# Optimization experiments

Measured on AMD Instinct MI355X. Metric: run time of the kernel, lower is better.

## Reference

```python
import jax, jax.numpy as jnp
import numpy as np

N_NODES = 50000
N_EDGES = 600000
F_IN = 64
N_GRAPHS = 2000
OUT_DIM = 1
BN_EPS = 1e-5


def _bn(x, gamma, beta):
    # BatchNorm1d training-mode forward: biased batch stats over node/row dim
    m = jnp.mean(x, axis=0)
    v = jnp.var(x, axis=0)
    return (x - m) * jax.lax.rsqrt(v + BN_EPS) * gamma + beta


def _gcn(x, W, b, src, dst):
    # PyG GCNConv: h = x @ W; symmetric-normalized aggregation with self-loops; bias after agg
    n = x.shape[0]
    h = x @ W                                    # [N, C_out]
    ones = jnp.ones((src.shape[0],), h.dtype)
    deg = jax.ops.segment_sum(ones, dst, num_segments=n) + 1.0  # +1 self-loop
    dinv = jax.lax.rsqrt(deg)
    norm = (dinv[src] * dinv[dst])[:, None]      # [E, 1]
    agg = jax.ops.segment_sum(h[src] * norm, dst, num_segments=n)
    agg = agg + h * (1.0 / deg)[:, None]         # self-loop term: deg^{-1/2}*deg^{-1/2}
    return agg + b


def _pool_mean(x, batch, g):
    s = jax.ops.segment_sum(x, batch, num_segments=g)
    c = jax.ops.segment_sum(jnp.ones((x.shape[0],), x.dtype), batch, num_segments=g)
    return s / jnp.maximum(c, 1.0)[:, None]


def _forward(xc, xs, W1c, b1c, g1c, be1c, W2c, b2c, g2c, be2c,
             W1s, b1s, g1s, be1s, W2s, b2s, g2s, be2s,
             Wf1, bf1, gf1, bef1, Wf2, bf2,
             src_c, dst_c, src_s, dst_s, batch):
    hc = jax.nn.relu(_bn(_gcn(xc, W1c, b1c, src_c, dst_c), g1c, be1c))
    hc = jax.nn.relu(_bn(_gcn(hc, W2c, b2c, src_c, dst_c), g2c, be2c))
    hs = jax.nn.relu(_bn(_gcn(xs, W1s, b1s, src_s, dst_s), g1s, be1s))
    hs = jax.nn.relu(_bn(_gcn(hs, W2s, b2s, src_s, dst_s), g2s, be2s))
    pc = _pool_mean(hc, batch, N_GRAPHS)         # [G, 64]
    ps = _pool_mean(hs, batch, N_GRAPHS)         # [G, 64]
    h = jnp.concatenate([pc, ps], axis=1)        # [G, 128]
    h = jax.nn.relu(_bn(h @ Wf1 + bf1, gf1, bef1))  # dropout is identity in eval
    return h @ Wf2 + bf2                         # [G, OUT_DIM]


def setup_inputs() -> dict:
    key = jax.random.key(0)
    ks = jax.random.split(key, 16)

    def glorot(k, fan_in, fan_out):
        s = np.sqrt(2.0 / (fan_in + fan_out)).astype(np.float32)
        return jax.random.normal(k, (fan_in, fan_out), jnp.float32) * s

    inp = {
        'x_chromophore': jax.random.normal(ks[0], (N_NODES, F_IN), jnp.float32),
        'x_solvent': jax.random.normal(ks[1], (N_NODES, F_IN), jnp.float32),
        'edge_index_chromophore': jax.random.randint(ks[2], (2, N_EDGES), 0, N_NODES),
        'edge_index_solvent': jax.random.randint(ks[3], (2, N_EDGES), 0, N_NODES),
        'batch': jnp.sort(jax.random.randint(ks[4], (N_NODES,), 0, N_GRAPHS)),
        # chromophore branch params
        'W1c': glorot(ks[5], F_IN, 128), 'b1c': jnp.zeros((128,), jnp.float32),
        'g1c': jnp.ones((128,), jnp.float32), 'be1c': jnp.zeros((128,), jnp.float32),
        'W2c': glorot(ks[6], 128, 64), 'b2c': jnp.zeros((64,), jnp.float32),
        'g2c': jnp.ones((64,), jnp.float32), 'be2c': jnp.zeros((64,), jnp.float32),
        # solvent branch params
        'W1s': glorot(ks[7], F_IN, 128), 'b1s': jnp.zeros((128,), jnp.float32),
        'g1s': jnp.ones((128,), jnp.float32), 'be1s': jnp.zeros((128,), jnp.float32),
        'W2s': glorot(ks[8], 128, 64), 'b2s': jnp.zeros((64,), jnp.float32),
        'g2s': jnp.ones((64,), jnp.float32), 'be2s': jnp.zeros((64,), jnp.float32),
        # MLP head
        'Wf1': glorot(ks[9], 128, 64), 'bf1': jnp.zeros((64,), jnp.float32),
        'gf1': jnp.ones((64,), jnp.float32), 'bef1': jnp.zeros((64,), jnp.float32),
        'Wf2': glorot(ks[10], 64, OUT_DIM), 'bf2': jnp.zeros((OUT_DIM,), jnp.float32),
    }
    return inp


def reference(x_chromophore, x_solvent, edge_index_chromophore, edge_index_solvent, batch,
              W1c, b1c, g1c, be1c, W2c, b2c, g2c, be2c,
              W1s, b1s, g1s, be1s, W2s, b2s, g2s, be2s,
              Wf1, bf1, gf1, bef1, Wf2, bf2):
    src_c, dst_c = edge_index_chromophore[0], edge_index_chromophore[1]
    src_s, dst_s = edge_index_solvent[0], edge_index_solvent[1]
    return _forward(x_chromophore, x_solvent,
                    W1c, b1c, g1c, be1c, W2c, b2c, g2c, be2c,
                    W1s, b1s, g1s, be1s, W2s, b2s, g2s, be2s,
                    Wf1, bf1, gf1, bef1, Wf2, bf2,
                    src_c, dst_c, src_s, dst_s, batch)
```

## Files before the change

### kernel.cpp

```cpp
#include <hip/hip_runtime.h>
#include <hip/hip_bf16.h>
#include <cstdint>
#include <cstddef>

#define NN 50000
#define NE 600000
#define NG 2000
#define NBUCK 49
#define SLOTS 16
#define NCHUNK 3125

typedef __attribute__((ext_vector_type(8))) short bf8;
typedef __attribute__((ext_vector_type(4))) float f32x4;

__device__ __forceinline__ unsigned short f2bf(float f) {
    uint32_t u = __float_as_uint(f);
    uint32_t r = (u + 0x7FFFu + ((u >> 16) & 1u)) >> 16;
    return (unsigned short)r;
}
__device__ __forceinline__ float bf2f(unsigned short h) {
    return __uint_as_float(((uint32_t)h) << 16);
}

__global__ __launch_bounds__(256) void conv_bf16_kernel(const float* __restrict__ x0,
                                                        const float* __restrict__ x1,
                                                        unsigned short* __restrict__ out) {
    int b = blockIdx.y;
    const float* x = b ? x1 : x0;
    unsigned short* o = out + (size_t)b * NN * 64;
    int i = (blockIdx.x * 256 + threadIdx.x) * 4;
    if (i + 3 < NN * 64) {
        float4 v = *(const float4*)&x[i];
        ushort4 r = make_ushort4(f2bf(v.x), f2bf(v.y), f2bf(v.z), f2bf(v.w));
        *(ushort4*)&o[i] = r;
    }
}

template<int K, int N>
__global__ __launch_bounds__(256) void pack_w(const float* __restrict__ W0,
                                              const float* __restrict__ W1,
                                              unsigned short* __restrict__ out) {
    int b = blockIdx.y;
    const float* W = b ? W1 : W0;
    unsigned short* o = out + (size_t)b * K * N;
    int idx = blockIdx.x * 256 + threadIdx.x;
    const int total = (N / 16) * (K / 32) * 64;
    if (idx >= total) return;
    int l = idx & 63;
    int th = idx >> 6;
    int h = th % (K / 32);
    int t = th / (K / 32);
    int col = t * 16 + (l & 15);
    int k0 = h * 32 + (l >> 4) * 8;
    ushort4 lo = make_ushort4(f2bf(W[(k0 + 0) * N + col]), f2bf(W[(k0 + 1) * N + col]),
                              f2bf(W[(k0 + 2) * N + col]), f2bf(W[(k0 + 3) * N + col]));
    ushort4 hi = make_ushort4(f2bf(W[(k0 + 4) * N + col]), f2bf(W[(k0 + 5) * N + col]),
                              f2bf(W[(k0 + 6) * N + col]), f2bf(W[(k0 + 7) * N + col]));
    *(ushort4*)&o[idx * 8] = lo;
    *(ushort4*)&o[idx * 8 + 4] = hi;
}

__global__ __launch_bounds__(256) void bucket_hist(const int* __restrict__ d0,
                                                   const int* __restrict__ d1,
                                                   int* __restrict__ bucketCnt, int nE) {
    int b = blockIdx.y;
    const int* dst = b ? d1 : d0;
    __shared__ int h[NBUCK];
    for (int i = threadIdx.x; i < NBUCK; i += 256) h[i] = 0;
    __syncthreads();
    for (int e = blockIdx.x * 256 + threadIdx.x; e < nE; e += gridDim.x * 256)
        atomicAdd(&h[dst[e] >> 10], 1);
    __syncthreads();
    for (int i = threadIdx.x; i < NBUCK; i += 256)
        if (h[i]) atomicAdd(&bucketCnt[b * NBUCK + i], h[i]);
}

__global__ void bucket_scan(const int* __restrict__ bucketCnt,
                            int* __restrict__ bucketOff, int* __restrict__ bucketCur) {
    int b = threadIdx.x;
    if (b < 2) {
        int run = 0;
        for (int i = 0; i < NBUCK; ++i) {
            bucketOff[b * NBUCK + i] = run;
            bucketCur[b * NBUCK + i] = run;
            run += bucketCnt[b * NBUCK + i];
        }
    }
}

__global__ __launch_bounds__(256) void bucket_scatter(const int* __restrict__ s0,
                                                      const int* __restrict__ d0,
                                                      const int* __restrict__ s1,
                                                      const int* __restrict__ d1,
                                                      int* __restrict__ bucketCur,
                                                      uint32_t* __restrict__ bent, int nE) {
    int b = blockIdx.y;
    const int* src = b ? s1 : s0;
    const int* dst = b ? d1 : d0;
    __shared__ int cnt[NBUCK];
    __shared__ int base[NBUCK];
    const int tid = threadIdx.x;
    for (int i = tid; i < NBUCK; i += 256) cnt[i] = 0;
    __syncthreads();

    const int e0 = blockIdx.x * 2048 + tid;
    int bk[8], slot[8];
    uint32_t pay[8];
#pragma unroll
    for (int k = 0; k < 8; ++k) {
        int e = e0 + k * 256;
        if (e < nE) {
            int d = dst[e], s = src[e];
            bk[k] = d >> 10;
            pay[k] = ((uint32_t)(d & 1023) << 16) | (uint32_t)s;
            slot[k] = atomicAdd(&cnt[bk[k]], 1);
        } else bk[k] = -1;
    }
    __syncthreads();
    for (int i = tid; i < NBUCK; i += 256) {
        int c = cnt[i];
        base[i] = c ? atomicAdd(&bucketCur[b * NBUCK + i], c) : 0;
    }
    __syncthreads();
#pragma unroll
    for (int k = 0; k < 8; ++k)
        if (bk[k] >= 0)
            bent[(size_t)b * NE + base[bk[k]] + slot[k]] = pay[k];
}

__global__ __launch_bounds__(256) void csr_build(const uint32_t* __restrict__ bent,
                                                 const int* __restrict__ bucketOff,
                                                 const int* __restrict__ bucketCnt,
                                                 int* __restrict__ row_ptr,
                                                 float* __restrict__ dinv,
                                                 uint16_t* __restrict__ perm) {
    __shared__ int lcnt[1024];
    __shared__ int lcur[1024];
    __shared__ int sscan[256];
    const int bk = blockIdx.x;
    const int b = blockIdx.y;
    const int tid = threadIdx.x;
    const int ebase = bucketOff[b * NBUCK + bk];
    const int ecnt = bucketCnt[b * NBUCK + bk];
    const int node0 = bk << 10;
    const uint32_t* be = bent + (size_t)b * NE + ebase;
    int* rp = row_ptr + b * (NN + 1);
    float* dv = dinv + (size_t)b * NN;
    uint16_t* pm = perm + (size_t)b * NE + ebase;

    for (int i = tid; i < 1024; i += 256) lcnt[i] = 0;
    __syncthreads();
    for (int i = tid; i < ecnt; i += 256) atomicAdd(&lcnt[be[i] >> 16], 1);
    __syncthreads();

    int c[4], s = 0;
#pragma unroll
    for (int j = 0; j < 4; ++j) { c[j] = lcnt[tid * 4 + j]; s += c[j]; }
    sscan[tid] = s;
    __syncthreads();
    for (int off = 1; off < 256; off <<= 1) {
        int v = (tid >= off) ? sscan[tid - off] : 0;
        __syncthreads();
        sscan[tid] += v;
        __syncthreads();
    }
    int run = sscan[tid] - s;
#pragma unroll
    for (int j = 0; j < 4; ++j) {
        int nl = tid * 4 + j;
        int g = node0 + nl;
        if (g < NN) {
            rp[g] = ebase + run;
            lcur[nl] = run;
            dv[g] = rsqrtf((float)c[j] + 1.0f);
        }
        run += c[j];
    }
    if (bk == NBUCK - 1 && tid == 0) rp[NN] = ebase + ecnt;
    __syncthreads();

    for (int i = tid; i < ecnt; i += 256) {
        uint32_t en = be[i];
        int nl = en >> 16;
        int pos = atomicAdd(&lcur[nl], 1);
        pm[pos] = (uint16_t)(en & 0xFFFFu);
    }
}

__global__ __launch_bounds__(256) void weight_fill(const uint16_t* __restrict__ perm,
                                                   const float* __restrict__ dinv,
                                                   uint32_t* __restrict__ permw, int nE) {
    int b = blockIdx.y;
    const uint16_t* pm = perm + (size_t)b * NE;
    const float* dv = dinv + (size_t)b * NN;
    uint32_t* pw = permw + (size_t)b * NE;
    int i = (blockIdx.x * 256 + threadIdx.x) * 4;
    if (i + 3 < nE) {
        ushort4 s4 = *(const ushort4*)&pm[i];
        uint4 o;
        o.x = ((uint32_t)f2bf(dv[s4.x]) << 16) | (uint32_t)s4.x;
        o.y = ((uint32_t)f2bf(dv[s4.y]) << 16) | (uint32_t)s4.y;
        o.z = ((uint32_t)f2bf(dv[s4.z]) << 16) | (uint32_t)s4.z;
        o.w = ((uint32_t)f2bf(dv[s4.w]) << 16) | (uint32_t)s4.w;
        *(uint4*)&pw[i] = o;
    } else {
        for (; i < nE; ++i) {
            uint16_t s = pm[i];
            pw[i] = ((uint32_t)f2bf(dv[s]) << 16) | (uint32_t)s;
        }
    }
}

template<bool STATS>
__global__ __launch_bounds__(256) void gemm1_mfma(const unsigned short* __restrict__ Xbf,
                                                  const unsigned short* __restrict__ Wp,
                                                  unsigned short* __restrict__ Y,
                                                  float* __restrict__ sums) {
    __shared__ float ls[128], ls2[128];
    const int b = blockIdx.y;
    const unsigned short* __restrict__ X = Xbf + (size_t)b * NN * 64;
    const unsigned short* __restrict__ W = Wp + (size_t)b * 64 * 128;
    unsigned short* __restrict__ Yb = Y + (size_t)b * NN * 128;
    const int tid = threadIdx.x;
    const int w = tid >> 6, lane = tid & 63;
    if (STATS) {
        for (int i = tid; i < 128; i += 256) { ls[i] = 0.f; ls2[i] = 0.f; }
        __syncthreads();
    }
    const int chunk = blockIdx.x * 4 + w;
    const bool act = chunk < NCHUNK;
    const int m = lane & 15, quad = lane >> 4;

    if (act) {
        const int row = chunk * 16 + m;
        bf8 a0 = *(const bf8*)&X[(size_t)row * 64 + quad * 8];
        bf8 a1 = *(const bf8*)&X[(size_t)row * 64 + 32 + quad * 8];
        f32x4 acc[8];
#pragma unroll
        for (int t = 0; t < 8; ++t) acc[t] = (f32x4){0.f, 0.f, 0.f, 0.f};
#pragma unroll
        for (int t = 0; t < 8; ++t) {
            bf8 b0 = *(const bf8*)&W[((t * 2 + 0) * 64 + lane) * 8];
            bf8 b1 = *(const bf8*)&W[((t * 2 + 1) * 64 + lane) * 8];
            acc[t] = __builtin_amdgcn_mfma_f32_16x16x32_bf16(a0, b0, acc[t], 0, 0, 0);
            acc[t] = __builtin_amdgcn_mfma_f32_16x16x32_bf16(a1, b1, acc[t], 0, 0, 0);
        }
        const int rbase = chunk * 16 + quad * 4;
#pragma unroll
        for (int t = 0; t < 8; ++t) {
            float s = 0.f, s2 = 0.f;
#pragma unroll
            for (int r = 0; r < 4; ++r) {
                float v = acc[t][r];
                Yb[(size_t)(rbase + r) * 128 + t * 16 + m] = f2bf(v);
                s += v; s2 = fmaf(v, v, s2);
            }
            if (STATS) {
                atomicAdd(&ls[t * 16 + m], s);
                atomicAdd(&ls2[t * 16 + m], s2);
            }
        }
    }
    if (STATS) {
        __syncthreads();
        int slot = blockIdx.x & (SLOTS - 1);
        float* sb = sums + (size_t)(b * SLOTS + slot) * 256;
        if (tid < 128) {
            atomicAdd(&sb[tid], ls[tid]);
            atomicAdd(&sb[128 + tid], ls2[tid]);
        }
    }
}

__global__ __launch_bounds__(256) void gemm2_mfma(const unsigned short* __restrict__ H1,
                                                  const unsigned short* __restrict__ Wp,
                                                  const float* __restrict__ scale,
                                                  const float* __restrict__ shift,
                                                  unsigned short* __restrict__ Y) {
    const int b = blockIdx.y;
    const unsigned short* __restrict__ X = H1 + (size_t)b * NN * 128;
    const unsigned short* __restrict__ W = Wp + (size_t)b * 128 * 64;
    const float* sc = scale + b * 128;
    const float* sh = shift + b * 128;
    unsigned short* __restrict__ Yb = Y + (size_t)b * NN * 64;
    const int tid = threadIdx.x;
    const int w = tid >> 6, lane = tid & 63;
    const int chunk = blockIdx.x * 4 + w;
    if (chunk >= NCHUNK) return;
    const int m = lane & 15, quad = lane >> 4;
    const int row = chunk * 16 + m;

    f32x4 acc[4];
#pragma unroll
    for (int t = 0; t < 4; ++t) acc[t] = (f32x4){0.f, 0.f, 0.f, 0.f};
#pragma unroll
    for (int h = 0; h < 4; ++h) {
        const int k0 = h * 32 + quad * 8;
        bf8 araw = *(const bf8*)&X[(size_t)row * 128 + k0];
        float4 sc0 = *(const float4*)&sc[k0];
        float4 sc1 = *(const float4*)&sc[k0 + 4];
        float4 sh0 = *(const float4*)&sh[k0];
        float4 sh1 = *(const float4*)&sh[k0 + 4];
        float scv[8] = {sc0.x, sc0.y, sc0.z, sc0.w, sc1.x, sc1.y, sc1.z, sc1.w};
        float shv[8] = {sh0.x, sh0.y, sh0.z, sh0.w, sh1.x, sh1.y, sh1.z, sh1.w};
        bf8 af;
#pragma unroll
        for (int j = 0; j < 8; ++j) {
            float v = bf2f((unsigned short)araw[j]);
            v = fmaxf(fmaf(v, scv[j], shv[j]), 0.f);
            af[j] = (short)f2bf(v);
        }
#pragma unroll
        for (int t = 0; t < 4; ++t) {
            bf8 bf = *(const bf8*)&W[((t * 4 + h) * 64 + lane) * 8];
            acc[t] = __builtin_amdgcn_mfma_f32_16x16x32_bf16(af, bf, acc[t], 0, 0, 0);
        }
    }
    const int rbase = chunk * 16 + quad * 4;
#pragma unroll
    for (int t = 0; t < 4; ++t)
#pragma unroll
        for (int r = 0; r < 4; ++r)
            Yb[(size_t)(rbase + r) * 64 + t * 16 + m] = f2bf(acc[t][r]);
}

template<bool STATS>
__global__ __launch_bounds__(256) void agg2_kernel(const unsigned short* __restrict__ hall,
                                                   const int* __restrict__ row_ptr,
                                                   const uint32_t* __restrict__ permw,
                                                   const float* __restrict__ dinv,
                                                   float* __restrict__ out,
                                                   float* __restrict__ sums, int nNodes) {
    const int b = blockIdx.y;
    const unsigned short* __restrict__ h = hall + (size_t)b * NN * 64;
    const int* rp = row_ptr + b * (NN + 1);
    const uint32_t* pe = permw + (size_t)b * NE;
    const float* dv = dinv + (size_t)b * NN;
    float* ob = out + (size_t)b * nNodes * 64;

    const int wave = blockIdx.x * 4 + (threadIdx.x >> 6);
    const int lane = threadIdx.x & 63;
    float fin = 0.f;
    const bool active = wave < nNodes;
    if (active) {
        const int d = wave;
        const float di = dv[d];
        const int p0 = rp[d], p1 = rp[d + 1];
        float a = 0.f;
        for (int p = p0; p < p1; p += 8) {
            int idx[8]; float w[8];
#pragma unroll
            for (int k = 0; k < 8; ++k) {
                bool vld = (p + k) < p1;
                int pk = vld ? (p + k) : p;
                uint32_t en = pe[pk];
                idx[k] = (int)(en & 0xFFFFu);
                w[k] = vld ? bf2f((unsigned short)(en >> 16)) : 0.f;
            }
            float v[8];
#pragma unroll
            for (int k = 0; k < 8; ++k) v[k] = bf2f(h[(size_t)idx[k] * 64 + lane]);
#pragma unroll
            for (int k = 0; k < 8; ++k) a = fmaf(w[k], v[k], a);
        }
        float hd = bf2f(h[(size_t)d * 64 + lane]);
        fin = di * fmaf(di, hd, a);
        ob[(size_t)d * 64 + lane] = fin;
    }
    if constexpr (STATS) {
        __shared__ float ls[256], ls2[256];
        ls[threadIdx.x] = fin;
        ls2[threadIdx.x] = fin * fin;
        __syncthreads();
        if (threadIdx.x < 64) {
            float s  = ls[threadIdx.x] + ls[threadIdx.x + 64] + ls[threadIdx.x + 128] + ls[threadIdx.x + 192];
            float s2 = ls2[threadIdx.x] + ls2[threadIdx.x + 64] + ls2[threadIdx.x + 128] + ls2[threadIdx.x + 192];
            int slot = blockIdx.x & (SLOTS - 1);
            float* sb = sums + ((size_t)(b * SLOTS + slot) * 2) * 64;
            atomicAdd(&sb[threadIdx.x], s);
            atomicAdd(&sb[64 + threadIdx.x], s2);
        }
    }
}

__global__ void bn_finalize2_kernel(const float* __restrict__ sums, int C, float invN,
                                    const float* __restrict__ g0, const float* __restrict__ g1,
                                    const float* __restrict__ b0, const float* __restrict__ b1,
                                    float* __restrict__ scale, float* __restrict__ shift) {
    int b = blockIdx.y;
    int c = threadIdx.x;
    if (c >= C) return;
    float s = 0.f, s2 = 0.f;
    for (int k = 0; k < SLOTS; ++k) {
        const float* sb = sums + ((size_t)(b * SLOTS + k) * 2) * C;
        s += sb[c];
        s2 += sb[C + c];
    }
    const float* gamma = b ? g1 : g0;
    const float* beta = b ? b1 : b0;
    float m = s * invN;
    float var = s2 * invN - m * m;
    float sc = gamma[c] * rsqrtf(var + 1e-5f);
    scale[b * C + c] = sc;
    shift[b * C + c] = beta[c] - m * sc;
}

__global__ void bn_finalize_kernel(const float* __restrict__ sums, int C, float invN,
                                   const float* __restrict__ gamma, const float* __restrict__ beta,
                                   float* __restrict__ scale, float* __restrict__ shift) {
    int c = blockIdx.x * blockDim.x + threadIdx.x;
    if (c >= C) return;
    float m = sums[c] * invN;
    float var = sums[C + c] * invN - m * m;
    float sc = gamma[c] * rsqrtf(var + 1e-5f);
    scale[c] = sc;
    shift[c] = beta[c] - m * sc;
}

__global__ __launch_bounds__(64) void pool2_kernel(const float* __restrict__ x,
                                                   const float* __restrict__ scale,
                                                   const float* __restrict__ shift,
                                                   const int* __restrict__ batch,
                                                   float* __restrict__ Hmean, int n) {
    int b = blockIdx.y;
    const float* xb = x + (size_t)b * NN * 64;
    int g = blockIdx.x;
    int c = threadIdx.x;
    int lo = 0, hi = n;
    while (lo < hi) { int mid = (lo + hi) >> 1; if (batch[mid] < g) lo = mid + 1; else hi = mid; }
    int start = lo;
    hi = n;
    while (lo < hi) { int mid = (lo + hi) >> 1; if (batch[mid] <= g) lo = mid + 1; else hi = mid; }
    int end = lo;
    float s = 0.f;
    float sc = scale[b * 64 + c], sh = shift[b * 64 + c];
    for (int r = start; r < end; ++r)
        s += fmaxf(fmaf(xb[(size_t)r * 64 + c], sc, sh), 0.f);
    float cf = (float)(end - start);
    Hmean[(size_t)g * 128 + b * 64 + c] = s / fmaxf(cf, 1.f);
}

__global__ __launch_bounds__(64) void head_gemm1_kernel(const float* __restrict__ H,
                                                        const float* __restrict__ Wf1,
                                                        float* __restrict__ T) {
    __shared__ float row[128];
    int g = blockIdx.x;
    int c = threadIdx.x;
    row[c] = H[(size_t)g * 128 + c];
    row[c + 64] = H[(size_t)g * 128 + 64 + c];
    __syncthreads();
    float acc = 0.f;
#pragma unroll 8
    for (int k = 0; k < 128; ++k) acc = fmaf(row[k], Wf1[k * 64 + c], acc);
    T[(size_t)g * 64 + c] = acc;
}

__global__ __launch_bounds__(64) void head_final_kernel(const float* __restrict__ T,
                                                        const float* __restrict__ scale,
                                                        const float* __restrict__ shift,
                                                        const float* __restrict__ Wf2,
                                                        const float* __restrict__ bf2,
                                                        float* __restrict__ out) {
    int g = blockIdx.x;
    int c = threadIdx.x;
    float v = fmaxf(fmaf(T[(size_t)g * 64 + c], scale[c], shift[c]), 0.f) * Wf2[c];
#pragma unroll
    for (int off = 32; off > 0; off >>= 1) v += __shfl_down(v, off, 64);
    if (c == 0) out[g] = v + bf2[0];
}

template<int C>
__global__ __launch_bounds__(256) void bn_stats_kernel(const float* __restrict__ x, int n,
                                                       float* __restrict__ sums) {
    constexpr int RP = 256 / C;
    __shared__ float ls[256], ls2[256];
    int c = threadIdx.x % C;
    int sub = threadIdx.x / C;
    float s = 0.f, s2 = 0.f;
    for (int r = blockIdx.x * RP + sub; r < n; r += gridDim.x * RP) {
        float v = x[(size_t)r * C + c];
        s += v; s2 += v * v;
    }
    ls[threadIdx.x] = s; ls2[threadIdx.x] = s2;
    __syncthreads();
    if (sub == 0) {
#pragma unroll
        for (int k = 1; k < RP; ++k) { s += ls[k * C + c]; s2 += ls2[k * C + c]; }
        atomicAdd(&sums[c], s);
        atomicAdd(&sums[C + c], s2);
    }
}


static inline size_t alignup(size_t x) { return (x + 255) & ~(size_t)255; }

extern "C" void kernel_launch(void* const* d_in, const int* in_sizes, int n_in,
                              void* d_out, int out_size, void* d_ws, size_t ws_size,
                              hipStream_t stream) {
    const float* xc  = (const float*)d_in[0];
    const float* xs  = (const float*)d_in[1];
    const int*   eic = (const int*)d_in[2];
    const int*   eis = (const int*)d_in[3];
    const int*   batch = (const int*)d_in[4];
    const float* W1c = (const float*)d_in[5];
    const float* g1c = (const float*)d_in[7];
    const float* be1c = (const float*)d_in[8];
    const float* W2c = (const float*)d_in[9];
    const float* g2c = (const float*)d_in[11];
    const float* be2c = (const float*)d_in[12];
    const float* W1s = (const float*)d_in[13];
    const float* g1s = (const float*)d_in[15];
    const float* be1s = (const float*)d_in[16];
    const float* W2s = (const float*)d_in[17];
    const float* g2s = (const float*)d_in[19];
    const float* be2s = (const float*)d_in[20];
    const float* Wf1 = (const float*)d_in[21];
    const float* gf1 = (const float*)d_in[23];
    const float* bef1 = (const float*)d_in[24];
    const float* Wf2 = (const float*)d_in[25];
    const float* bf2 = (const float*)d_in[26];
    float* out = (float*)d_out;

    char* ws = (char*)d_ws;
    size_t off = 0;
    auto alloc = [&](size_t bytes) { char* p = ws + off; off += alignup(bytes); return p; };

    int*      bucketCnt = (int*)alloc(2 * NBUCK * 4);
    int*      bucketOff = (int*)alloc(2 * NBUCK * 4);
    int*      bucketCur = (int*)alloc(2 * NBUCK * 4);
    uint32_t* bent      = (uint32_t*)alloc((size_t)2 * NE * 4);
    uint16_t* perm      = (uint16_t*)alloc(((size_t)2 * NE + 64) * 2);
    int*      row_ptr   = (int*)alloc(2 * (NN + 1) * 4);
    float*    dinv      = (float*)alloc((size_t)2 * NN * 4);
    unsigned short* xbf   = (unsigned short*)alloc((size_t)2 * NN * 64 * 2);
    unsigned short* h1bf  = (unsigned short*)alloc((size_t)2 * NN * 128 * 2);
    unsigned short* h2bf  = (unsigned short*)alloc((size_t)2 * NN * 64 * 2);
    unsigned short* Wp1   = (unsigned short*)alloc((size_t)2 * 64 * 128 * 2);
    unsigned short* Wp2   = (unsigned short*)alloc((size_t)2 * 128 * 64 * 2);
    float*    aggx      = (float*)alloc((size_t)2 * NN * 64 * 4);
    float*    sums      = (float*)alloc((size_t)2 * SLOTS * 2 * 128 * 4);
    float*    hsums     = (float*)alloc(128 * 4);
    float*    bnscale   = (float*)alloc(2 * 128 * 4);
    float*    bnshift   = (float*)alloc(2 * 128 * 4);
    float*    Hmean     = (float*)alloc((size_t)NG * 128 * 4);
    float*    T         = (float*)alloc((size_t)NG * 64 * 4);

    const float invN = 1.0f / (float)NN;
    const size_t sumsBytes = (size_t)2 * SLOTS * 2 * 128 * 4;
    const int gemmBlocks = (NCHUNK + 3) / 4;

    conv_bf16_kernel<<<dim3((NN * 64 / 4 + 255) / 256, 2), 256, 0, stream>>>(xc, xs, xbf);
    pack_w<64, 128><<<dim3(4, 2), 256, 0, stream>>>(W1c, W1s, Wp1);
    pack_w<128, 64><<<dim3(4, 2), 256, 0, stream>>>(W2c, W2s, Wp2);

    hipMemsetAsync(bucketCnt, 0, 2 * NBUCK * 4, stream);
    bucket_hist<<<dim3(64, 2), 256, 0, stream>>>(eic + NE, eis + NE, bucketCnt, NE);
    bucket_scan<<<1, 64, 0, stream>>>(bucketCnt, bucketOff, bucketCur);
    bucket_scatter<<<dim3((NE + 2047) / 2048, 2), 256, 0, stream>>>(
        eic, eic + NE, eis, eis + NE, bucketCur, bent, NE);
    csr_build<<<dim3(NBUCK, 2), 256, 0, stream>>>(bent, bucketOff, bucketCnt,
                                                  row_ptr, dinv, perm);
    weight_fill<<<dim3((NE / 4 + 255) / 256, 2), 256, 0, stream>>>(perm, dinv, bent, NE);

    agg2_kernel<false><<<dim3((NN + 3) / 4, 2), 256, 0, stream>>>(
        xbf, row_ptr, bent, dinv, aggx, nullptr, NN);
    conv_bf16_kernel<<<dim3((NN * 64 / 4 + 255) / 256, 2), 256, 0, stream>>>(
        aggx, aggx + (size_t)NN * 64, xbf);
    hipMemsetAsync(sums, 0, sumsBytes, stream);
    gemm1_mfma<true><<<dim3(gemmBlocks, 2), 256, 0, stream>>>(xbf, Wp1, h1bf, sums);
    bn_finalize2_kernel<<<dim3(1, 2), 128, 0, stream>>>(sums, 128, invN,
                                                        g1c, g1s, be1c, be1s, bnscale, bnshift);

    gemm2_mfma<<<dim3(gemmBlocks, 2), 256, 0, stream>>>(h1bf, Wp2, bnscale, bnshift, h2bf);
    hipMemsetAsync(sums, 0, sumsBytes, stream);
    agg2_kernel<true><<<dim3((NN + 3) / 4, 2), 256, 0, stream>>>(
        h2bf, row_ptr, bent, dinv, aggx, sums, NN);
    bn_finalize2_kernel<<<dim3(1, 2), 64, 0, stream>>>(sums, 64, invN,
                                                       g2c, g2s, be2c, be2s, bnscale, bnshift);

    pool2_kernel<<<dim3(NG, 2), 64, 0, stream>>>(aggx, bnscale, bnshift, batch, Hmean, NN);

    head_gemm1_kernel<<<NG, 64, 0, stream>>>(Hmean, Wf1, T);
    hipMemsetAsync(hsums, 0, 128 * 4, stream);
    bn_stats_kernel<64><<<32, 256, 0, stream>>>(T, NG, hsums);
    bn_finalize_kernel<<<1, 64, 0, stream>>>(hsums, 64, 1.0f / (float)NG, gf1, bef1,
                                             bnscale, bnshift);
    head_final_kernel<<<NG, 64, 0, stream>>>(T, bnscale, bnshift, Wf2, bf2, out);
}
```

Baseline: 409.1 us.

## Vectorize edge aggregation with 4-edge lanes and write bf16 output directly

The aggregation kernel now has each 16-lane group handle one edge, loading 4 bf16 features per lane (8-byte loads), and reduces the partial sums across groups with shuffles. It writes bf16 output directly, which removes the separate fp32-to-bf16 conversion kernel and halves the aggregation output and pool input traffic. The BN stats memsets are merged into a single upfront memset, and the per-block reduction uses LDS atomics. Storing the second-layer aggregate in bf16 before BN and pooling adds rounding error.

After: 423.4 us. +3.5%, slower.

```diff
diff --git a/kernel.cpp b/kernel.cpp
--- a/kernel.cpp
+++ b/kernel.cpp
@@ -21,6 +21,8 @@
 __device__ __forceinline__ float bf2f(unsigned short h) {
     return __uint_as_float(((uint32_t)h) << 16);
 }
+__device__ __forceinline__ float bflo(uint32_t u) { return __uint_as_float(u << 16); }
+__device__ __forceinline__ float bfhi(uint32_t u) { return __uint_as_float(u & 0xFFFF0000u); }
 
 __global__ __launch_bounds__(256) void conv_bf16_kernel(const float* __restrict__ x0,
                                                         const float* __restrict__ x1,
@@ -325,60 +327,82 @@
 }
 
 template<bool STATS>
-__global__ __launch_bounds__(256) void agg2_kernel(const unsigned short* __restrict__ hall,
+__global__ __launch_bounds__(256) void agg3_kernel(const unsigned short* __restrict__ hall,
                                                    const int* __restrict__ row_ptr,
                                                    const uint32_t* __restrict__ permw,
                                                    const float* __restrict__ dinv,
-                                                   float* __restrict__ out,
+                                                   unsigned short* __restrict__ out,
                                                    float* __restrict__ sums, int nNodes) {
     const int b = blockIdx.y;
     const unsigned short* __restrict__ h = hall + (size_t)b * NN * 64;
     const int* rp = row_ptr + b * (NN + 1);
     const uint32_t* pe = permw + (size_t)b * NE;
     const float* dv = dinv + (size_t)b * NN;
-    float* ob = out + (size_t)b * nNodes * 64;
+    unsigned short* ob = out + (size_t)b * nNodes * 64;
 
     const int wave = blockIdx.x * 4 + (threadIdx.x >> 6);
     const int lane = threadIdx.x & 63;
-    float fin = 0.f;
+    const int g = lane >> 4;
+    const int li = lane & 15;
+    float fin0 = 0.f, fin1 = 0.f, fin2 = 0.f, fin3 = 0.f;
     const bool active = wave < nNodes;
     if (active) {
         const int d = wave;
         const float di = dv[d];
         const int p0 = rp[d], p1 = rp[d + 1];
-        float a = 0.f;
+        float a0 = 0.f, a1 = 0.f, a2 = 0.f, a3 = 0.f;
         for (int p = p0; p < p1; p += 8) {
-            int idx[8]; float w[8];
-#pragma unroll
-            for (int k = 0; k < 8; ++k) {
-                bool vld = (p + k) < p1;
-                int pk = vld ? (p + k) : p;
+#pragma unroll
+            for (int q = 0; q < 2; ++q) {
+                int pk = p + q * 4 + g;
+                bool vld = pk < p1;
+                pk = vld ? pk : p0;
                 uint32_t en = pe[pk];
-                idx[k] = (int)(en & 0xFFFFu);
-                w[k] = vld ? bf2f((unsigned short)(en >> 16)) : 0.f;
+                int idx = (int)(en & 0xFFFFu);
+                float w = vld ? bf2f((unsigned short)(en >> 16)) : 0.f;
+                uint2 hv = *(const uint2*)&h[(size_t)idx * 64 + li * 4];
+                a0 = fmaf(w, bflo(hv.x), a0);
+                a1 = fmaf(w, bfhi(hv.x), a1);
+                a2 = fmaf(w, bflo(hv.y), a2);
+                a3 = fmaf(w, bfhi(hv.y), a3);
             }
-            float v[8];
-#pragma unroll
-            for (int k = 0; k < 8; ++k) v[k] = bf2f(h[(size_t)idx[k] * 64 + lane]);
-#pragma unroll
-            for (int k = 0; k < 8; ++k) a = fmaf(w[k], v[k], a);
-        }
-        float hd = bf2f(h[(size_t)d * 64 + lane]);
-        fin = di * fmaf(di, hd, a);
-        ob[(size_t)d * 64 + lane] = fin;
+        }
+        uint2 hd = *(const uint2*)&h[(size_t)d * 64 + li * 4];
+        float ws = (g == 0) ? di : 0.f;
+        a0 = fmaf(ws, bflo(hd.x), a0);
+        a1 = fmaf(ws, bfhi(hd.x), a1);
+        a2 = fmaf(ws, bflo(hd.y), a2);
+        a3 = fmaf(ws, bfhi(hd.y), a3);
+        a0 += __shfl_xor(a0, 16, 64); a0 += __shfl_xor(a0, 32, 64);
+        a1 += __shfl_xor(a1, 16, 64); a1 += __shfl_xor(a1, 32, 64);
+        a2 += __shfl_xor(a2, 16, 64); a2 += __shfl_xor(a2, 32, 64);
+        a3 += __shfl_xor(a3, 16, 64); a3 += __shfl_xor(a3, 32, 64);
+        fin0 = di * a0; fin1 = di * a1; fin2 = di * a2; fin3 = di * a3;
+        if (g == 0) {
+            ushort4 st = make_ushort4(f2bf(fin0), f2bf(fin1), f2bf(fin2), f2bf(fin3));
+            *(ushort4*)&ob[(size_t)d * 64 + li * 4] = st;
+        }
     }
     if constexpr (STATS) {
-        __shared__ float ls[256], ls2[256];
-        ls[threadIdx.x] = fin;
-        ls2[threadIdx.x] = fin * fin;
+        __shared__ float ls[64], ls2[64];
+        if (threadIdx.x < 64) { ls[threadIdx.x] = 0.f; ls2[threadIdx.x] = 0.f; }
+        __syncthreads();
+        if (active && g == 0) {
+            atomicAdd(&ls[li * 4 + 0], fin0);
+            atomicAdd(&ls[li * 4 + 1], fin1);
+            atomicAdd(&ls[li * 4 + 2], fin2);
+            atomicAdd(&ls[li * 4 + 3], fin3);
+            atomicAdd(&ls2[li * 4 + 0], fin0 * fin0);
+            atomicAdd(&ls2[li * 4 + 1], fin1 * fin1);
+            atomicAdd(&ls2[li * 4 + 2], fin2 * fin2);
+            atomicAdd(&ls2[li * 4 + 3], fin3 * fin3);
+        }
         __syncthreads();
         if (threadIdx.x < 64) {
-            float s  = ls[threadIdx.x] + ls[threadIdx.x + 64] + ls[threadIdx.x + 128] + ls[threadIdx.x + 192];
-            float s2 = ls2[threadIdx.x] + ls2[threadIdx.x + 64] + ls2[threadIdx.x + 128] + ls2[threadIdx.x + 192];
             int slot = blockIdx.x & (SLOTS - 1);
             float* sb = sums + ((size_t)(b * SLOTS + slot) * 2) * 64;
-            atomicAdd(&sb[threadIdx.x], s);
-            atomicAdd(&sb[64 + threadIdx.x], s2);
+            atomicAdd(&sb[threadIdx.x], ls[threadIdx.x]);
+            atomicAdd(&sb[64 + threadIdx.x], ls2[threadIdx.x]);
         }
     }
 }
@@ -417,13 +441,13 @@
     shift[c] = beta[c] - m * sc;
 }
 
-__global__ __launch_bounds__(64) void pool2_kernel(const float* __restrict__ x,
+__global__ __launch_bounds__(64) void pool2_kernel(const unsigned short* __restrict__ x,
                                                    const float* __restrict__ scale,
                                                    const float* __restrict__ shift,
                                                    const int* __restrict__ batch,
                                                    float* __restrict__ Hmean, int n) {
     int b = blockIdx.y;
-    const float* xb = x + (size_t)b * NN * 64;
+    const unsigned short* xb = x + (size_t)b * NN * 64;
     int g = blockIdx.x;
     int c = threadIdx.x;
     int lo = 0, hi = n;
@@ -435,7 +459,7 @@
     float s = 0.f;
     float sc = scale[b * 64 + c], sh = shift[b * 64 + c];
     for (int r = start; r < end; ++r)
-        s += fmaxf(fmaf(xb[(size_t)r * 64 + c], sc, sh), 0.f);
+        s += fmaxf(fmaf(bf2f(xb[(size_t)r * 64 + c]), sc, sh), 0.f);
     float cf = (float)(end - start);
     Hmean[(size_t)g * 128 + b * 64 + c] = s / fmaxf(cf, 1.f);
 }
@@ -533,25 +557,28 @@
     int*      row_ptr   = (int*)alloc(2 * (NN + 1) * 4);
     float*    dinv      = (float*)alloc((size_t)2 * NN * 4);
     unsigned short* xbf   = (unsigned short*)alloc((size_t)2 * NN * 64 * 2);
+    unsigned short* aggbf = (unsigned short*)alloc((size_t)2 * NN * 64 * 2);
     unsigned short* h1bf  = (unsigned short*)alloc((size_t)2 * NN * 128 * 2);
     unsigned short* h2bf  = (unsigned short*)alloc((size_t)2 * NN * 64 * 2);
     unsigned short* Wp1   = (unsigned short*)alloc((size_t)2 * 64 * 128 * 2);
     unsigned short* Wp2   = (unsigned short*)alloc((size_t)2 * 128 * 64 * 2);
-    float*    aggx      = (float*)alloc((size_t)2 * NN * 64 * 4);
-    float*    sums      = (float*)alloc((size_t)2 * SLOTS * 2 * 128 * 4);
-    float*    hsums     = (float*)alloc(128 * 4);
+    float*    sums1     = (float*)alloc(((size_t)2 * SLOTS * 256 + (size_t)2 * SLOTS * 128 + 128) * 4);
+    float*    sums2     = sums1 + (size_t)2 * SLOTS * 256;
+    float*    hsums     = sums2 + (size_t)2 * SLOTS * 128;
     float*    bnscale   = (float*)alloc(2 * 128 * 4);
     float*    bnshift   = (float*)alloc(2 * 128 * 4);
     float*    Hmean     = (float*)alloc((size_t)NG * 128 * 4);
     float*    T         = (float*)alloc((size_t)NG * 64 * 4);
 
     const float invN = 1.0f / (float)NN;
-    const size_t sumsBytes = (size_t)2 * SLOTS * 2 * 128 * 4;
+    const size_t statBytes = ((size_t)2 * SLOTS * 256 + (size_t)2 * SLOTS * 128 + 128) * 4;
     const int gemmBlocks = (NCHUNK + 3) / 4;
+    const int aggBlocks = NN / 4;
 
     conv_bf16_kernel<<<dim3((NN * 64 / 4 + 255) / 256, 2), 256, 0, stream>>>(xc, xs, xbf);
     pack_w<64, 128><<<dim3(4, 2), 256, 0, stream>>>(W1c, W1s, Wp1);
     pack_w<128, 64><<<dim3(4, 2), 256, 0, stream>>>(W2c, W2s, Wp2);
+    hipMemsetAsync(sums1, 0, statBytes, stream);
 
     hipMemsetAsync(bucketCnt, 0, 2 * NBUCK * 4, stream);
     bucket_hist<<<dim3(64, 2), 256, 0, stream>>>(eic + NE, eis + NE, bucketCnt, NE);
@@ -562,26 +589,21 @@
                                                   row_ptr, dinv, perm);
     weight_fill<<<dim3((NE / 4 + 255) / 256, 2), 256, 0, stream>>>(perm, dinv, bent, NE);
 
-    agg2_kernel<false><<<dim3((NN + 3) / 4, 2), 256, 0, stream>>>(
-        xbf, row_ptr, bent, dinv, aggx, nullptr, NN);
-    conv_bf16_kernel<<<dim3((NN * 64 / 4 + 255) / 256, 2), 256, 0, stream>>>(
-        aggx, aggx + (size_t)NN * 64, xbf);
-    hipMemsetAsync(sums, 0, sumsBytes, stream);
-    gemm1_mfma<true><<<dim3(gemmBlocks, 2), 256, 0, stream>>>(xbf, Wp1, h1bf, sums);
-    bn_finalize2_kernel<<<dim3(1, 2), 128, 0, stream>>>(sums, 128, invN,
+    agg3_kernel<false><<<dim3(aggBlocks, 2), 256, 0, stream>>>(
+        xbf, row_ptr, bent, dinv, aggbf, nullptr, NN);
+    gemm1_mfma<true><<<dim3(gemmBlocks, 2), 256, 0, stream>>>(aggbf, Wp1, h1bf, sums1);
+    bn_finalize2_kernel<<<dim3(1, 2), 128, 0, stream>>>(sums1, 128, invN,
                                                         g1c, g1s, be1c, be1s, bnscale, bnshift);
 
     gemm2_mfma<<<dim3(gemmBlocks, 2), 256, 0, stream>>>(h1bf, Wp2, bnscale, bnshift, h2bf);
-    hipMemsetAsync(sums, 0, sumsBytes, stream);
-    agg2_kernel<true><<<dim3((NN + 3) / 4, 2), 256, 0, stream>>>(
-        h2bf, row_ptr, bent, dinv, aggx, sums, NN);
-    bn_finalize2_kernel<<<dim3(1, 2), 64, 0, stream>>>(sums, 64, invN,
+    agg3_kernel<true><<<dim3(aggBlocks, 2), 256, 0, stream>>>(
+        h2bf, row_ptr, bent, dinv, aggbf, sums2, NN);
+    bn_finalize2_kernel<<<dim3(1, 2), 64, 0, stream>>>(sums2, 64, invN,
                                                        g2c, g2s, be2c, be2s, bnscale, bnshift);
 
-    pool2_kernel<<<dim3(NG, 2), 64, 0, stream>>>(aggx, bnscale, bnshift, batch, Hmean, NN);
+    pool2_kernel<<<dim3(NG, 2), 64, 0, stream>>>(aggbf, bnscale, bnshift, batch, Hmean, NN);
 
     head_gemm1_kernel<<<NG, 64, 0, stream>>>(Hmean, Wf1, T);
-    hipMemsetAsync(hsums, 0, 128 * 4, stream);
     bn_stats_kernel<64><<<32, 256, 0, stream>>>(T, NG, hsums);
     bn_finalize_kernel<<<1, 64, 0, stream>>>(hsums, 64, 1.0f / (float)NG, gf1, bef1,
                                              bnscale, bnshift);
```
